# Kernel tuning notes

Measured on AMD Instinct MI355X. Metric: run time of the kernel, lower is better.

The kernel has to match this reference:

```python
import jax, jax.numpy as jnp
import numpy as np

B, N, H = 128, 2048, 128
FEAT = 15


def setup_inputs() -> dict:
    key = jax.random.key(0)
    ks = jax.random.split(key, 24)
    f32 = jnp.float32
    inp = {
        'x':   jax.random.normal(ks[0], (B, N), f32),
        'x1':  jax.random.uniform(ks[1], (B, N), f32),
        'x2':  jax.random.uniform(ks[2], (B, N), f32),
        'z1':  jax.random.uniform(ks[3], (B, N), f32),
        'z2':  jax.random.uniform(ks[4], (B, N), f32),
        'x1E': jax.random.uniform(ks[5], (B, N), f32),
        'x2E': jax.random.uniform(ks[6], (B, N), f32),
        'z1E': jax.random.uniform(ks[7], (B, N), f32),
        'z2E': jax.random.uniform(ks[8], (B, N), f32),
        'muB': jax.random.uniform(ks[9], (B, 1), f32, 0.01, 0.1),
        'lb':  jax.random.normal(ks[10], (B, N), f32) - 2.0,
        'ub':  jax.random.normal(ks[11], (B, N), f32) + 2.0,
        'has_lb': jnp.ones((B, N), bool),
        'has_ub': jnp.ones((B, N), bool),
        # LSTM params (PyTorch gate order i, f, g, o)
        'W_ih': 0.1 * jax.random.normal(ks[12], (4 * H, FEAT), f32),
        'W_hh': 0.1 * jax.random.normal(ks[13], (4 * H, H), f32),
        'b_ih': 0.1 * jax.random.normal(ks[14], (4 * H,), f32),
        'b_hh': 0.1 * jax.random.normal(ks[15], (4 * H,), f32),
        # px_head: Linear(H,H) -> ReLU -> Linear(H,1)
        'W1': 0.1 * jax.random.normal(ks[16], (H, H), f32),
        'b1': 0.1 * jax.random.normal(ks[17], (H,), f32),
        'W2': 0.1 * jax.random.normal(ks[18], (1, H), f32),
        'b2': 0.1 * jax.random.normal(ks[19], (1,), f32),
    }
    return inp


def _forward(x, x1, x2, z1, z2, x1E, x2E, z1E, z2E, muB, lb, ub,
             W_ih, W_hh, b_ih, b_hh, W1, b1, W2, b2, has_lb, has_ub):
    Bb, n = x.shape
    eps = 1e-12
    # slack / bad-coordinate handling
    z1 = jnp.where((z1 + muB) <= 0, 0.0, z1)
    z2 = jnp.where((z2 + muB) <= 0, 0.0, z2)
    # quadratic merit stand-in: M = 0.5(||x||^2 + ||z1||^2 + ||z2||^2)
    grad_x, grad_z1, grad_z2 = x, z1, z2
    invD1 = jnp.clip((z1 + muB) / (x1 + muB + eps), 0.0, 100.0)
    invD2 = jnp.clip((z2 + muB) / (x2 + muB + eps), 0.0, 100.0)
    muB_bn = jnp.broadcast_to(muB, (Bb, n))
    # [B, n, 15] -> [B*n, 15]
    feat = jnp.stack([x, x1, x2, z1, z2, grad_x, grad_z1, grad_z2,
                      x1E, x2E, z1E, z2E, muB_bn, invD1, invD2], axis=-1)
    feat = feat.reshape(Bb * n, FEAT)
    # single-step LSTM cell, h0 = c0 = 0 so W_hh @ h0 vanishes
    gates = feat @ W_ih.T + b_ih + b_hh          # [B*n, 4H]
    i, f, g, o = jnp.split(gates, 4, axis=-1)
    c = jax.nn.sigmoid(i) * jnp.tanh(g)
    h = jax.nn.sigmoid(o) * jnp.tanh(c)          # [B*n, H]
    # MLP head -> per-coordinate positive step size
    p = jax.nn.relu(h @ W1.T + b1) @ W2.T + b2   # [B*n, 1]
    p_x = jnp.abs(p).reshape(Bb, n)
    # elementwise updates
    d_x = -p_x * grad_x
    x_new = x + d_x
    z1 = z1 - invD1 * (-p_x * grad_x + grad_z1)
    z2 = z2 - invD2 * (p_x * grad_x + grad_z2)
    x = x_new  # project_step = identity accept
    x1 = jnp.where(has_lb, x - lb, 0.0)
    x2 = jnp.where(has_ub, ub - x, 0.0)
    return jnp.concatenate([x, x1, x2, z1, z2], axis=-1)  # [B, 5n]


def reference(x, x1, x2, z1, z2, x1E, x2E, z1E, z2E, muB, lb, ub,
              has_lb, has_ub, W_ih, W_hh, b_ih, b_hh, W1, b1, W2, b2):
    return _forward(x, x1, x2, z1, z2, x1E, x2E, z1E, z2E, muB, lb, ub,
                    W_ih, W_hh, b_ih, b_hh, W1, b1, W2, b2, has_lb, has_ub)
```

## Files before the change

### kernel.cpp

```cpp
#include <hip/hip_runtime.h>


typedef _Float16 half4v  __attribute__((ext_vector_type(4)));
typedef _Float16 half8v  __attribute__((ext_vector_type(8)));
typedef float    float4v __attribute__((ext_vector_type(4)));

#define N_SZ   2048
#define ROWS   262144
#define BLOCKT 256
#define MTILE  64
#define ITERS  4
#define NBLK   (ROWS / (MTILE * ITERS))

#define FS 24
#define HS 136

__device__ __forceinline__ float fast_rcp(float x) { return __builtin_amdgcn_rcpf(x); }
__device__ __forceinline__ float sigm(float x)  { return fast_rcp(1.0f + __expf(-x)); }
__device__ __forceinline__ float tanh_f(float x){ return 1.0f - 2.0f * fast_rcp(1.0f + __expf(2.0f * x)); }

__global__ __launch_bounds__(BLOCKT)
void ps_lstm_mfma(const float* __restrict__ x_,
                  const float* __restrict__ x1_,
                  const float* __restrict__ x2_,
                  const float* __restrict__ z1_,
                  const float* __restrict__ z2_,
                  const float* __restrict__ x1E_,
                  const float* __restrict__ x2E_,
                  const float* __restrict__ z1E_,
                  const float* __restrict__ z2E_,
                  const float* __restrict__ muB_,
                  const float* __restrict__ lb_,
                  const float* __restrict__ ub_,
                  const float* __restrict__ Wih_,
                  const float* __restrict__ bih_,
                  const float* __restrict__ bhh_,
                  const float* __restrict__ W1_,
                  const float* __restrict__ b1_,
                  const float* __restrict__ W2_,
                  const float* __restrict__ b2_,
                  float* __restrict__ out_)
{
    __shared__ __align__(16) _Float16 sWihT[384 * FS];
    __shared__ __align__(16) _Float16 sW1T [128 * FS * 0 + 128 * HS];
    __shared__ __align__(16) _Float16 sFeat[MTILE * FS];
    __shared__ __align__(16) _Float16 sH   [MTILE * HS];
    __shared__ float sGB[3][128];
    __shared__ float sB1[128];
    __shared__ float sW2[128];
    __shared__ float sPp[4][MTILE];

    const int tid  = threadIdx.x;
    const int lane = tid & 63;
    const int w    = tid >> 6;
    const int c    = lane & 15;
    const int q    = lane >> 4;

    for (int n3 = tid; n3 < 384; n3 += BLOCKT) {
        const int grow = n3 + (n3 >= 128 ? 128 : 0);
        #pragma unroll
        for (int k = 0; k < 15; ++k)
            sWihT[n3 * FS + k] = (_Float16)Wih_[grow * 15 + k];
        sWihT[n3 * FS + 15] = (_Float16)0.f;
        sGB[n3 >> 7][n3 & 127] = bih_[grow] + bhh_[grow];
    }
    for (int idx = tid; idx < 128 * 128; idx += BLOCKT) {
        const int nn = idx >> 7, k = idx & 127;
        sW1T[nn * HS + k] = (_Float16)W1_[nn * 128 + k];
    }
    for (int i = tid; i < 128; i += BLOCKT) { sB1[i] = b1_[i]; sW2[i] = W2_[i]; }
    const float b2v = b2_[0];

    float ex = 0.f, ez1 = 0.f, ez2 = 0.f, eD1 = 0.f, eD2 = 0.f, elb = 0.f, eub = 0.f;
    int   erow = 0;

    for (int it = 0; it < ITERS; ++it) {
        const int tile  = blockIdx.x * ITERS + it;
        const int rbase = tile * MTILE;

        if (tid < MTILE) {
            const int r = rbase + tid;
            const float x   = x_[r];
            const float x1  = x1_[r];
            const float x2  = x2_[r];
            float       z1  = z1_[r];
            float       z2  = z2_[r];
            const float x1E = x1E_[r];
            const float x2E = x2E_[r];
            const float z1E = z1E_[r];
            const float z2E = z2E_[r];
            const float mu  = muB_[r >> 11];

            z1 = ((z1 + mu) <= 0.0f) ? 0.0f : z1;
            z2 = ((z2 + mu) <= 0.0f) ? 0.0f : z2;
            float invD1 = (z1 + mu) * fast_rcp(x1 + mu + 1e-12f);
            float invD2 = (z2 + mu) * fast_rcp(x2 + mu + 1e-12f);
            invD1 = fminf(fmaxf(invD1, 0.0f), 100.0f);
            invD2 = fminf(fmaxf(invD2, 0.0f), 100.0f);

            const float f[15] = { x, x1, x2, z1, z2, x, z1, z2,
                                  x1E, x2E, z1E, z2E, mu, invD1, invD2 };
            _Float16* fr = &sFeat[tid * FS];
            #pragma unroll
            for (int k = 0; k < 15; ++k) fr[k] = (_Float16)f[k];
            fr[15] = (_Float16)0.f;

            ex = x; ez1 = z1; ez2 = z2; eD1 = invD1; eD2 = invD2;
            elb = lb_[r]; eub = ub_[r]; erow = r;
        }
        __syncthreads();

        {
            const half8v zf = {(_Float16)0.f,(_Float16)0.f,(_Float16)0.f,(_Float16)0.f,
                               (_Float16)0.f,(_Float16)0.f,(_Float16)0.f,(_Float16)0.f};
            half8v af[4];
            #pragma unroll
            for (int m = 0; m < 4; ++m) {
                af[m] = zf;
                if (q < 2)
                    af[m] = *(const half8v*)&sFeat[(m * 16 + c) * FS + q * 8];
            }
            #pragma unroll
            for (int nn = 0; nn < 2; ++nn) {
                const int nt = w * 2 + nn;
                half8v bi = zf, bg = zf, bo = zf;
                if (q < 2) {
                    bi = *(const half8v*)&sWihT[(0 * 128 + nt * 16 + c) * FS + q * 8];
                    bg = *(const half8v*)&sWihT[(1 * 128 + nt * 16 + c) * FS + q * 8];
                    bo = *(const half8v*)&sWihT[(2 * 128 + nt * 16 + c) * FS + q * 8];
                }
                const float bib = sGB[0][nt * 16 + c];
                const float bgb = sGB[1][nt * 16 + c];
                const float bob = sGB[2][nt * 16 + c];

                float4v di[4], dg[4], dv[4];
                const float4v zc = {0.f, 0.f, 0.f, 0.f};
                #pragma unroll
                for (int m = 0; m < 4; ++m) {
                    di[m] = __builtin_amdgcn_mfma_f32_16x16x32_f16(af[m], bi, zc, 0, 0, 0);
                    dg[m] = __builtin_amdgcn_mfma_f32_16x16x32_f16(af[m], bg, zc, 0, 0, 0);
                    dv[m] = __builtin_amdgcn_mfma_f32_16x16x32_f16(af[m], bo, zc, 0, 0, 0);
                }
                #pragma unroll
                for (int m = 0; m < 4; ++m) {
                    #pragma unroll
                    for (int j = 0; j < 4; ++j) {
                        const float ipre = di[m][j] + bib;
                        const float gpre = dg[m][j] + bgb;
                        const float opre = dv[m][j] + bob;
                        const float cv   = sigm(ipre) * tanh_f(gpre);
                        const float hv   = sigm(opre) * tanh_f(cv);
                        sH[(m * 16 + q * 4 + j) * HS + nt * 16 + c] = (_Float16)hv;
                    }
                }
            }
        }
        __syncthreads();

        {
            float4v acc[2][4];
            #pragma unroll
            for (int nn = 0; nn < 2; ++nn)
                #pragma unroll
                for (int m = 0; m < 4; ++m)
                    acc[nn][m] = (float4v){0.f, 0.f, 0.f, 0.f};

            #pragma unroll
            for (int kk = 0; kk < 4; ++kk) {
                half8v ah[4];
                #pragma unroll
                for (int m = 0; m < 4; ++m)
                    ah[m] = *(const half8v*)&sH[(m * 16 + c) * HS + kk * 32 + q * 8];
                #pragma unroll
                for (int nn = 0; nn < 2; ++nn) {
                    const int nt = w * 2 + nn;
                    const half8v bh = *(const half8v*)&sW1T[(nt * 16 + c) * HS + kk * 32 + q * 8];
                    #pragma unroll
                    for (int m = 0; m < 4; ++m)
                        acc[nn][m] = __builtin_amdgcn_mfma_f32_16x16x32_f16(ah[m], bh, acc[nn][m], 0, 0, 0);
                }
            }

            float part[4][4];
            #pragma unroll
            for (int m = 0; m < 4; ++m)
                #pragma unroll
                for (int j = 0; j < 4; ++j) part[m][j] = 0.f;

            #pragma unroll
            for (int nn = 0; nn < 2; ++nn) {
                const int nt  = w * 2 + nn;
                const float bb = sB1[nt * 16 + c];
                const float ww = sW2[nt * 16 + c];
                #pragma unroll
                for (int m = 0; m < 4; ++m)
                    #pragma unroll
                    for (int j = 0; j < 4; ++j)
                        part[m][j] = __builtin_fmaf(fmaxf(acc[nn][m][j] + bb, 0.f), ww, part[m][j]);
            }
            #pragma unroll
            for (int m = 0; m < 4; ++m)
                #pragma unroll
                for (int j = 0; j < 4; ++j) {
                    float v = part[m][j];
                    v += __shfl_xor(v, 1, 64);
                    v += __shfl_xor(v, 2, 64);
                    v += __shfl_xor(v, 4, 64);
                    v += __shfl_xor(v, 8, 64);
                    part[m][j] = v;
                }
            if (c == 0) {
                #pragma unroll
                for (int m = 0; m < 4; ++m)
                    #pragma unroll
                    for (int j = 0; j < 4; ++j)
                        sPp[w][m * 16 + q * 4 + j] = part[m][j];
            }
        }
        __syncthreads();

        if (tid < MTILE) {
            const float p   = sPp[0][tid] + sPp[1][tid] + sPp[2][tid] + sPp[3][tid] + b2v;
            const float p_x = fabsf(p);
            const int   b   = erow >> 11;
            const int   n   = erow & (N_SZ - 1);
            const float pxx   = p_x * ex;
            const float x_new = ex - pxx;
            float* ob = out_ + (size_t)b * (5 * N_SZ) + n;
            ob[0 * N_SZ] = x_new;
            ob[1 * N_SZ] = x_new - elb;
            ob[2 * N_SZ] = eub - x_new;
            ob[3 * N_SZ] = ez1 - eD1 * (ez1 - pxx);
            ob[4 * N_SZ] = ez2 - eD2 * (ez2 + pxx);
        }
    }
}

extern "C" void kernel_launch(void* const* d_in, const int* in_sizes, int n_in,
                              void* d_out, int out_size, void* d_ws, size_t ws_size,
                              hipStream_t stream) {
    (void)in_sizes; (void)n_in; (void)out_size; (void)d_ws; (void)ws_size;
    const float* x_   = (const float*)d_in[0];
    const float* x1_  = (const float*)d_in[1];
    const float* x2_  = (const float*)d_in[2];
    const float* z1_  = (const float*)d_in[3];
    const float* z2_  = (const float*)d_in[4];
    const float* x1E_ = (const float*)d_in[5];
    const float* x2E_ = (const float*)d_in[6];
    const float* z1E_ = (const float*)d_in[7];
    const float* z2E_ = (const float*)d_in[8];
    const float* muB_ = (const float*)d_in[9];
    const float* lb_  = (const float*)d_in[10];
    const float* ub_  = (const float*)d_in[11];
    const float* Wih_ = (const float*)d_in[14];
    const float* bih_ = (const float*)d_in[16];
    const float* bhh_ = (const float*)d_in[17];
    const float* W1_  = (const float*)d_in[18];
    const float* b1_  = (const float*)d_in[19];
    const float* W2_  = (const float*)d_in[20];
    const float* b2_  = (const float*)d_in[21];
    float* out_ = (float*)d_out;

    ps_lstm_mfma<<<NBLK, BLOCKT, 0, stream>>>(
        x_, x1_, x2_, z1_, z2_, x1E_, x2E_, z1E_, z2E_, muB_, lb_, ub_,
        Wih_, bih_, bhh_, W1_, b1_, W2_, b2_, out_);
}
```

Measured before the change: 166.4 us.

## Give each wave its own row tiles so the main loop needs no block barriers

Each wavefront now owns 32-row tiles and runs the whole pipeline for them: feature build, gate MFMAs, LSTM activations, a chunked hidden stage through a small per-wave LDS buffer, the W1 MFMAs and the head reduction. This removes the three block-wide __syncthreads per tile and interleaves the two GEMMs in 32-column chunks. Gate biases and head weights now live in registers, W1 is loaded with vectorized float4 reads, and tanh of the cell state uses a polynomial. The costs are higher register pressure, since there are 16 float4 accumulators per wave. The per-wave buffers also rely on implicit wave-level ordering of LDS writes and reads, and the polynomial tanh is only accurate on a bounded input range.

After: 144.6 us. 1.15x faster.

```diff
diff --git a/kernel.cpp b/kernel.cpp
--- a/kernel.cpp
+++ b/kernel.cpp
@@ -1,54 +1,56 @@
 #include <hip/hip_runtime.h>
 
 
-typedef _Float16 half4v  __attribute__((ext_vector_type(4)));
 typedef _Float16 half8v  __attribute__((ext_vector_type(8)));
 typedef float    float4v __attribute__((ext_vector_type(4)));
 
 #define N_SZ   2048
 #define ROWS   262144
 #define BLOCKT 256
-#define MTILE  64
-#define ITERS  4
-#define NBLK   (ROWS / (MTILE * ITERS))
+#define NBLK   512
+#define WITERS 4
+#define WROWS  32
 
 #define FS 24
 #define HS 136
+#define SS 40
 
 __device__ __forceinline__ float fast_rcp(float x) { return __builtin_amdgcn_rcpf(x); }
 __device__ __forceinline__ float sigm(float x)  { return fast_rcp(1.0f + __expf(-x)); }
 __device__ __forceinline__ float tanh_f(float x){ return 1.0f - 2.0f * fast_rcp(1.0f + __expf(2.0f * x)); }
-
-__global__ __launch_bounds__(BLOCKT)
-void ps_lstm_mfma(const float* __restrict__ x_,
-                  const float* __restrict__ x1_,
-                  const float* __restrict__ x2_,
-                  const float* __restrict__ z1_,
-                  const float* __restrict__ z2_,
-                  const float* __restrict__ x1E_,
-                  const float* __restrict__ x2E_,
-                  const float* __restrict__ z1E_,
-                  const float* __restrict__ z2E_,
-                  const float* __restrict__ muB_,
-                  const float* __restrict__ lb_,
-                  const float* __restrict__ ub_,
-                  const float* __restrict__ Wih_,
-                  const float* __restrict__ bih_,
-                  const float* __restrict__ bhh_,
-                  const float* __restrict__ W1_,
-                  const float* __restrict__ b1_,
-                  const float* __restrict__ W2_,
-                  const float* __restrict__ b2_,
-                  float* __restrict__ out_)
+__device__ __forceinline__ float tanh_c(float y) {
+    const float t = y * y;
+    return y * __builtin_fmaf(t, __builtin_fmaf(t, __builtin_fmaf(t,
+            -0.02714f, 0.12052f), -0.33157f), 0.99986f);
+}
+
+__global__ __launch_bounds__(BLOCKT, 2)
+void ps_lstm_wfree(const float* __restrict__ x_,
+                   const float* __restrict__ x1_,
+                   const float* __restrict__ x2_,
+                   const float* __restrict__ z1_,
+                   const float* __restrict__ z2_,
+                   const float* __restrict__ x1E_,
+                   const float* __restrict__ x2E_,
+                   const float* __restrict__ z1E_,
+                   const float* __restrict__ z2E_,
+                   const float* __restrict__ muB_,
+                   const float* __restrict__ lb_,
+                   const float* __restrict__ ub_,
+                   const float* __restrict__ Wih_,
+                   const float* __restrict__ bih_,
+                   const float* __restrict__ bhh_,
+                   const float* __restrict__ W1_,
+                   const float* __restrict__ b1_,
+                   const float* __restrict__ W2_,
+                   const float* __restrict__ b2_,
+                   float* __restrict__ out_)
 {
     __shared__ __align__(16) _Float16 sWihT[384 * FS];
-    __shared__ __align__(16) _Float16 sW1T [128 * FS * 0 + 128 * HS];
-    __shared__ __align__(16) _Float16 sFeat[MTILE * FS];
-    __shared__ __align__(16) _Float16 sH   [MTILE * HS];
-    __shared__ float sGB[3][128];
-    __shared__ float sB1[128];
-    __shared__ float sW2[128];
-    __shared__ float sPp[4][MTILE];
+    __shared__ __align__(16) _Float16 sW1T [128 * HS];
+    __shared__ __align__(16) _Float16 sFeat[4][WROWS * FS];
+    __shared__ __align__(16) _Float16 sHs  [4][WROWS * SS];
+    __shared__ float sP[4][WROWS];
 
     const int tid  = threadIdx.x;
     const int lane = tid & 63;
@@ -62,24 +64,47 @@
         for (int k = 0; k < 15; ++k)
             sWihT[n3 * FS + k] = (_Float16)Wih_[grow * 15 + k];
         sWihT[n3 * FS + 15] = (_Float16)0.f;
-        sGB[n3 >> 7][n3 & 127] = bih_[grow] + bhh_[grow];
-    }
-    for (int idx = tid; idx < 128 * 128; idx += BLOCKT) {
-        const int nn = idx >> 7, k = idx & 127;
-        sW1T[nn * HS + k] = (_Float16)W1_[nn * 128 + k];
-    }
-    for (int i = tid; i < 128; i += BLOCKT) { sB1[i] = b1_[i]; sW2[i] = W2_[i]; }
+    }
+    {
+        const int n  = tid >> 1;
+        const int hf = tid & 1;
+        const float4* src = (const float4*)(W1_ + n * 128 + hf * 64);
+        #pragma unroll
+        for (int v = 0; v < 16; v += 2) {
+            const float4 a = src[v];
+            const float4 bq = src[v + 1];
+            half8v hh;
+            hh[0] = (_Float16)a.x;  hh[1] = (_Float16)a.y;
+            hh[2] = (_Float16)a.z;  hh[3] = (_Float16)a.w;
+            hh[4] = (_Float16)bq.x; hh[5] = (_Float16)bq.y;
+            hh[6] = (_Float16)bq.z; hh[7] = (_Float16)bq.w;
+            *(half8v*)&sW1T[n * HS + hf * 64 + v * 4] = hh;
+        }
+    }
+
+    float bi[8], bg[8], bo[8], b1r[8], w2r[8];
+    #pragma unroll
+    for (int nt = 0; nt < 8; ++nt) {
+        const int nb = nt * 16 + c;
+        bi[nt]  = bih_[nb]       + bhh_[nb];
+        bg[nt]  = bih_[256 + nb] + bhh_[256 + nb];
+        bo[nt]  = bih_[384 + nb] + bhh_[384 + nb];
+        b1r[nt] = b1_[nb];
+        w2r[nt] = W2_[nb];
+    }
     const float b2v = b2_[0];
 
-    float ex = 0.f, ez1 = 0.f, ez2 = 0.f, eD1 = 0.f, eD2 = 0.f, elb = 0.f, eub = 0.f;
-    int   erow = 0;
-
-    for (int it = 0; it < ITERS; ++it) {
-        const int tile  = blockIdx.x * ITERS + it;
-        const int rbase = tile * MTILE;
-
-        if (tid < MTILE) {
-            const int r = rbase + tid;
+    __syncthreads();
+
+    const int gw = blockIdx.x * 4 + w;
+
+    #pragma unroll 1
+    for (int it = 0; it < WITERS; ++it) {
+        const int rbase = (gw * WITERS + it) * WROWS;
+
+        float ex = 0.f, ez1 = 0.f, ez2 = 0.f, eD1 = 0.f, eD2 = 0.f, elb = 0.f, eub = 0.f;
+        if (lane < WROWS) {
+            const int r = rbase + lane;
             const float x   = x_[r];
             const float x1  = x1_[r];
             const float x2  = x2_[r];
@@ -100,131 +125,113 @@
 
             const float f[15] = { x, x1, x2, z1, z2, x, z1, z2,
                                   x1E, x2E, z1E, z2E, mu, invD1, invD2 };
-            _Float16* fr = &sFeat[tid * FS];
-            #pragma unroll
-            for (int k = 0; k < 15; ++k) fr[k] = (_Float16)f[k];
-            fr[15] = (_Float16)0.f;
+            half8v f0, f1;
+            #pragma unroll
+            for (int k = 0; k < 8; ++k) f0[k] = (_Float16)f[k];
+            #pragma unroll
+            for (int k = 0; k < 7; ++k) f1[k] = (_Float16)f[8 + k];
+            f1[7] = (_Float16)0.f;
+            *(half8v*)&sFeat[w][lane * FS]     = f0;
+            *(half8v*)&sFeat[w][lane * FS + 8] = f1;
 
             ex = x; ez1 = z1; ez2 = z2; eD1 = invD1; eD2 = invD2;
-            elb = lb_[r]; eub = ub_[r]; erow = r;
-        }
-        __syncthreads();
-
-        {
-            const half8v zf = {(_Float16)0.f,(_Float16)0.f,(_Float16)0.f,(_Float16)0.f,
-                               (_Float16)0.f,(_Float16)0.f,(_Float16)0.f,(_Float16)0.f};
-            half8v af[4];
-            #pragma unroll
-            for (int m = 0; m < 4; ++m) {
-                af[m] = zf;
-                if (q < 2)
-                    af[m] = *(const half8v*)&sFeat[(m * 16 + c) * FS + q * 8];
-            }
-            #pragma unroll
-            for (int nn = 0; nn < 2; ++nn) {
-                const int nt = w * 2 + nn;
-                half8v bi = zf, bg = zf, bo = zf;
+            elb = lb_[r]; eub = ub_[r];
+        }
+
+        half8v fA[2];
+        #pragma unroll
+        for (int m = 0; m < 2; ++m) {
+            half8v z8;
+            #pragma unroll
+            for (int k = 0; k < 8; ++k) z8[k] = (_Float16)0.f;
+            fA[m] = (q < 2) ? *(const half8v*)&sFeat[w][(m * 16 + c) * FS + q * 8] : z8;
+        }
+
+        float4v acc[8][2];
+        #pragma unroll
+        for (int nt = 0; nt < 8; ++nt)
+            #pragma unroll
+            for (int m = 0; m < 2; ++m)
+                acc[nt][m] = (float4v){0.f, 0.f, 0.f, 0.f};
+
+        #pragma unroll
+        for (int kk = 0; kk < 4; ++kk) {
+            #pragma unroll
+            for (int nt2 = 0; nt2 < 2; ++nt2) {
+                const int nt = kk * 2 + nt2;
+                half8v Bi, Bg, Bo;
+                #pragma unroll
+                for (int k = 0; k < 8; ++k) { Bi[k] = (_Float16)0.f; Bg[k] = (_Float16)0.f; Bo[k] = (_Float16)0.f; }
                 if (q < 2) {
-                    bi = *(const half8v*)&sWihT[(0 * 128 + nt * 16 + c) * FS + q * 8];
-                    bg = *(const half8v*)&sWihT[(1 * 128 + nt * 16 + c) * FS + q * 8];
-                    bo = *(const half8v*)&sWihT[(2 * 128 + nt * 16 + c) * FS + q * 8];
+                    const int nb = nt * 16 + c;
+                    Bi = *(const half8v*)&sWihT[(nb)*FS       + q * 8];
+                    Bg = *(const half8v*)&sWihT[(128 + nb)*FS + q * 8];
+                    Bo = *(const half8v*)&sWihT[(256 + nb)*FS + q * 8];
                 }
-                const float bib = sGB[0][nt * 16 + c];
-                const float bgb = sGB[1][nt * 16 + c];
-                const float bob = sGB[2][nt * 16 + c];
-
-                float4v di[4], dg[4], dv[4];
-                const float4v zc = {0.f, 0.f, 0.f, 0.f};
-                #pragma unroll
-                for (int m = 0; m < 4; ++m) {
-                    di[m] = __builtin_amdgcn_mfma_f32_16x16x32_f16(af[m], bi, zc, 0, 0, 0);
-                    dg[m] = __builtin_amdgcn_mfma_f32_16x16x32_f16(af[m], bg, zc, 0, 0, 0);
-                    dv[m] = __builtin_amdgcn_mfma_f32_16x16x32_f16(af[m], bo, zc, 0, 0, 0);
-                }
-                #pragma unroll
-                for (int m = 0; m < 4; ++m) {
+                #pragma unroll
+                for (int m = 0; m < 2; ++m) {
+                    const float4v zc = {0.f, 0.f, 0.f, 0.f};
+                    float4v di = __builtin_amdgcn_mfma_f32_16x16x32_f16(fA[m], Bi, zc, 0, 0, 0);
+                    float4v dg = __builtin_amdgcn_mfma_f32_16x16x32_f16(fA[m], Bg, zc, 0, 0, 0);
+                    float4v dv = __builtin_amdgcn_mfma_f32_16x16x32_f16(fA[m], Bo, zc, 0, 0, 0);
                     #pragma unroll
                     for (int j = 0; j < 4; ++j) {
-                        const float ipre = di[m][j] + bib;
-                        const float gpre = dg[m][j] + bgb;
-                        const float opre = dv[m][j] + bob;
-                        const float cv   = sigm(ipre) * tanh_f(gpre);
-                        const float hv   = sigm(opre) * tanh_f(cv);
-                        sH[(m * 16 + q * 4 + j) * HS + nt * 16 + c] = (_Float16)hv;
+                        const float cv = sigm(di[j] + bi[nt]) * tanh_f(dg[j] + bg[nt]);
+                        const float hv = sigm(dv[j] + bo[nt]) * tanh_c(cv);
+                        sHs[w][(m * 16 + q * 4 + j) * SS + nt2 * 16 + c] = (_Float16)hv;
                     }
                 }
             }
-        }
-        __syncthreads();
-
-        {
-            float4v acc[2][4];
-            #pragma unroll
-            for (int nn = 0; nn < 2; ++nn)
-                #pragma unroll
-                for (int m = 0; m < 4; ++m)
-                    acc[nn][m] = (float4v){0.f, 0.f, 0.f, 0.f};
-
-            #pragma unroll
-            for (int kk = 0; kk < 4; ++kk) {
-                half8v ah[4];
-                #pragma unroll
-                for (int m = 0; m < 4; ++m)
-                    ah[m] = *(const half8v*)&sH[(m * 16 + c) * HS + kk * 32 + q * 8];
-                #pragma unroll
-                for (int nn = 0; nn < 2; ++nn) {
-                    const int nt = w * 2 + nn;
-                    const half8v bh = *(const half8v*)&sW1T[(nt * 16 + c) * HS + kk * 32 + q * 8];
-                    #pragma unroll
-                    for (int m = 0; m < 4; ++m)
-                        acc[nn][m] = __builtin_amdgcn_mfma_f32_16x16x32_f16(ah[m], bh, acc[nn][m], 0, 0, 0);
-                }
+            half8v hA[2];
+            #pragma unroll
+            for (int m = 0; m < 2; ++m)
+                hA[m] = *(const half8v*)&sHs[w][(m * 16 + c) * SS + q * 8];
+            #pragma unroll
+            for (int nt = 0; nt < 8; ++nt) {
+                const half8v Bh = *(const half8v*)&sW1T[(nt * 16 + c) * HS + kk * 32 + q * 8];
+                #pragma unroll
+                for (int m = 0; m < 2; ++m)
+                    acc[nt][m] = __builtin_amdgcn_mfma_f32_16x16x32_f16(hA[m], Bh, acc[nt][m], 0, 0, 0);
             }
-
-            float part[4][4];
-            #pragma unroll
-            for (int m = 0; m < 4; ++m)
-                #pragma unroll
-                for (int j = 0; j < 4; ++j) part[m][j] = 0.f;
-
-            #pragma unroll
-            for (int nn = 0; nn < 2; ++nn) {
-                const int nt  = w * 2 + nn;
-                const float bb = sB1[nt * 16 + c];
-                const float ww = sW2[nt * 16 + c];
-                #pragma unroll
-                for (int m = 0; m < 4; ++m)
-                    #pragma unroll
-                    for (int j = 0; j < 4; ++j)
-                        part[m][j] = __builtin_fmaf(fmaxf(acc[nn][m][j] + bb, 0.f), ww, part[m][j]);
+        }
+
+        float part[2][4];
+        #pragma unroll
+        for (int m = 0; m < 2; ++m)
+            #pragma unroll
+            for (int j = 0; j < 4; ++j) part[m][j] = 0.f;
+        #pragma unroll
+        for (int nt = 0; nt < 8; ++nt)
+            #pragma unroll
+            for (int m = 0; m < 2; ++m)
+                #pragma unroll
+                for (int j = 0; j < 4; ++j)
+                    part[m][j] = __builtin_fmaf(fmaxf(acc[nt][m][j] + b1r[nt], 0.f),
+                                                w2r[nt], part[m][j]);
+        #pragma unroll
+        for (int m = 0; m < 2; ++m)
+            #pragma unroll
+            for (int j = 0; j < 4; ++j) {
+                float v = part[m][j];
+                v += __shfl_xor(v, 1, 64);
+                v += __shfl_xor(v, 2, 64);
+                v += __shfl_xor(v, 4, 64);
+                v += __shfl_xor(v, 8, 64);
+                part[m][j] = v;
             }
-            #pragma unroll
-            for (int m = 0; m < 4; ++m)
-                #pragma unroll
-                for (int j = 0; j < 4; ++j) {
-                    float v = part[m][j];
-                    v += __shfl_xor(v, 1, 64);
-                    v += __shfl_xor(v, 2, 64);
-                    v += __shfl_xor(v, 4, 64);
-                    v += __shfl_xor(v, 8, 64);
-                    part[m][j] = v;
-                }
-            if (c == 0) {
-                #pragma unroll
-                for (int m = 0; m < 4; ++m)
-                    #pragma unroll
-                    for (int j = 0; j < 4; ++j)
-                        sPp[w][m * 16 + q * 4 + j] = part[m][j];
-            }
-        }
-        __syncthreads();
-
-        if (tid < MTILE) {
-            const float p   = sPp[0][tid] + sPp[1][tid] + sPp[2][tid] + sPp[3][tid] + b2v;
-            const float p_x = fabsf(p);
-            const int   b   = erow >> 11;
-            const int   n   = erow & (N_SZ - 1);
-            const float pxx   = p_x * ex;
+        if (c == 0) {
+            #pragma unroll
+            for (int m = 0; m < 2; ++m)
+                #pragma unroll
+                for (int j = 0; j < 4; ++j)
+                    sP[w][m * 16 + q * 4 + j] = part[m][j];
+        }
+        if (lane < WROWS) {
+            const int   r     = rbase + lane;
+            const int   b     = r >> 11;
+            const int   n     = r & (N_SZ - 1);
+            const float p     = sP[w][lane] + b2v;
+            const float pxx   = fabsf(p) * ex;
             const float x_new = ex - pxx;
             float* ob = out_ + (size_t)b * (5 * N_SZ) + n;
             ob[0 * N_SZ] = x_new;
@@ -261,7 +268,7 @@
     const float* b2_  = (const float*)d_in[21];
     float* out_ = (float*)d_out;
 
-    ps_lstm_mfma<<<NBLK, BLOCKT, 0, stream>>>(
+    ps_lstm_wfree<<<NBLK, BLOCKT, 0, stream>>>(
         x_, x1_, x2_, z1_, z2_, x1E_, x2E_, z1E_, z2E_, muB_, lb_, ub_,
         Wih_, bih_, bhh_, W1_, b1_, W2_, b2_, out_);
 }
```
